# Kernel optimization log

Hardware: AMD Instinct MI355X
Metric: run time of the kernel (lower is better)

## Reference

```python
import jax, jax.numpy as jnp
import numpy as np

EMB = 1024
HID = 4096
NHEADS = 16
DK = EMB // NHEADS
EPS = 1e-6
B, S = 2, 2048


def setup_inputs() -> dict:
    key = jax.random.key(0)
    ks = jax.random.split(key, 10)
    sc = 0.02
    return {
        "x": jax.random.normal(ks[0], (B, S, EMB), dtype=jnp.float32),
        "src_mask": jnp.ones((B, 1, 1, S), dtype=jnp.int32),
        "wq": jax.random.normal(ks[1], (EMB, EMB), dtype=jnp.float32) * sc,
        "wk": jax.random.normal(ks[2], (EMB, EMB), dtype=jnp.float32) * sc,
        "wv": jax.random.normal(ks[3], (EMB, EMB), dtype=jnp.float32) * sc,
        "wo": jax.random.normal(ks[4], (EMB, EMB), dtype=jnp.float32) * sc,
        "ff1_w": jax.random.normal(ks[5], (EMB, HID), dtype=jnp.float32) * sc,
        "ff1_b": jnp.zeros((HID,), dtype=jnp.float32),
        "ff2_w": jax.random.normal(ks[6], (HID, EMB), dtype=jnp.float32) * sc,
        "ff2_b": jnp.zeros((EMB,), dtype=jnp.float32),
        "ln1_a": jnp.ones((1,), dtype=jnp.float32),
        "ln1_b": jnp.zeros((1,), dtype=jnp.float32),
        "ln2_a": jnp.ones((1,), dtype=jnp.float32),
        "ln2_b": jnp.zeros((1,), dtype=jnp.float32),
    }


def layernorm(x, alpha, bias):
    # Faithful to the custom LayerNorm: scalar alpha/bias, std with Bessel
    # correction (torch default unbiased=True), divide by (std + eps).
    mean = jnp.mean(x, axis=-1, keepdims=True)
    var = jnp.sum((x - mean) ** 2, axis=-1, keepdims=True) / (x.shape[-1] - 1)
    std = jnp.sqrt(var)
    return alpha * (x - mean) / (std + EPS) + bias


def mha(x, mask, wq, wk, wv, wo):
    b, s, _ = x.shape
    def split_heads(t):  # [B,S,E] -> [B,H,S,dk]
        return t.reshape(b, s, NHEADS, DK).transpose(0, 2, 1, 3)
    q = split_heads(x @ wq)
    k = split_heads(x @ wk)
    v = split_heads(x @ wv)
    scores = jnp.einsum("bhqd,bhkd->bhqk", q, k) / jnp.sqrt(jnp.float32(DK))
    scores = jnp.where(mask == 0, -jnp.inf, scores)
    attn = jax.nn.softmax(scores, axis=-1)
    out = jnp.einsum("bhqk,bhkd->bhqd", attn, v)
    out = out.transpose(0, 2, 1, 3).reshape(b, s, EMB)
    return out @ wo


def ffn(x, w1, b1, w2, b2):
    return jax.nn.relu(x @ w1 + b1) @ w2 + b2


def reference(x, src_mask, wq, wk, wv, wo, ff1_w, ff1_b, ff2_w, ff2_b,
              ln1_a, ln1_b, ln2_a, ln2_b):
    # pre-norm residual encoder block (dropout=0 / eval mode)
    h = x + mha(layernorm(x, ln1_a, ln1_b), src_mask, wq, wk, wv, wo)
    out = h + ffn(layernorm(h, ln2_a, ln2_b), ff1_w, ff1_b, ff2_w, ff2_b)
    return out
```

## Files before the change

kernel.cpp:

```cpp
#include <hip/hip_runtime.h>
#include <stdint.h>

#define EMB 1024
#define HID 4096
#define NHEADS 16
#define DKH 64
#define SEQ 2048
#define BATCH 2
#define MROWS (BATCH * SEQ)
#define GBK 64

typedef unsigned short u16;
typedef unsigned int u32;
typedef __attribute__((ext_vector_type(8))) short short8;
typedef __attribute__((ext_vector_type(4))) float f32x4;
typedef __attribute__((ext_vector_type(16))) float f32x16;
typedef __attribute__((ext_vector_type(4))) u32 u32x4;
typedef __attribute__((ext_vector_type(2))) int i32x2;

#if __has_builtin(__builtin_amdgcn_exp2f)
#define QK_SCALE 0.18033688011f
#define QK_CLAMP 43.3f
__device__ __forceinline__ float pexp(float x) { return __builtin_amdgcn_exp2f(x); }
#else
#define QK_SCALE 0.125f
#define QK_CLAMP 30.0f
__device__ __forceinline__ float pexp(float x) { return __expf(x); }
#endif

__device__ __forceinline__ u16 f2bf(float f) {
    unsigned u = __float_as_uint(f);
    unsigned r = 0x7FFFu + ((u >> 16) & 1u);
    return (u16)((u + r) >> 16);
}
__device__ __forceinline__ f32x4 mfma16(short8 a, short8 b, f32x4 c) {
    return __builtin_amdgcn_mfma_f32_16x16x32_bf16(a, b, c, 0, 0, 0);
}
__device__ __forceinline__ f32x16 mfma32(short8 a, short8 b, f32x16 c) {
    return __builtin_amdgcn_mfma_f32_32x32x16_bf16(a, b, c, 0, 0, 0);
}
__device__ __forceinline__ void gl_lds16(const u16* g, u16* l) {
    __builtin_amdgcn_global_load_lds(
        (__attribute__((address_space(1))) void*)g,
        (__attribute__((address_space(3))) void*)l, 16, 0, 0);
}
__device__ __forceinline__ void plswap(u32& a, u32& b) {
#if __has_builtin(__builtin_amdgcn_permlane32_swap)
    i32x2 r = __builtin_amdgcn_permlane32_swap((int)a, (int)b, false, false);
    a = (u32)r.x; b = (u32)r.y;
#else
    const u32 ta = (u32)__shfl_xor((int)a, 32);
    const u32 tb = (u32)__shfl_xor((int)b, 32);
    const bool hi = (threadIdx.x & 32) != 0;
    const u32 na = hi ? tb : a;
    const u32 nb = hi ? b : ta;
    a = na; b = nb;
#endif
}
__device__ __forceinline__ short8 mk8(u32 a, u32 b, u32 c, u32 d) {
    u32x4 t; t.x = a; t.y = b; t.z = c; t.w = d;
    return __builtin_bit_cast(short8, t);
}

__global__ __launch_bounds__(256) void transpose_qkvo(
    const float* __restrict__ wq, const float* __restrict__ wk,
    const float* __restrict__ wv, const float* __restrict__ wo,
    u16* __restrict__ qkvT, u16* __restrict__ woT,
    const int* __restrict__ msk, int* __restrict__ flag) {
    __shared__ u16 t[32][33];
    const int z = blockIdx.z;
    const float* W = (z == 0) ? wq : (z == 1) ? wk : (z == 2) ? wv : wo;
    u16* WT = (z < 3) ? (qkvT + (size_t)z * EMB * EMB) : woT;
    const float scale = (z == 0) ? QK_SCALE : 1.0f;
    const int tx = threadIdx.x & 31, ty = threadIdx.x >> 5;
    const int k0 = blockIdx.y * 32, n0 = blockIdx.x * 32;
#pragma unroll
    for (int r = 0; r < 32; r += 8)
        t[ty + r][tx] = f2bf(scale * W[(size_t)(k0 + ty + r) * EMB + n0 + tx]);
    __syncthreads();
#pragma unroll
    for (int r = 0; r < 32; r += 8)
        WT[(size_t)(n0 + ty + r) * EMB + k0 + tx] = t[tx][ty + r];

    if (z == 3 && blockIdx.x == 0 && blockIdx.y == 0) {
        int v = 1;
        for (int i = threadIdx.x; i < BATCH * SEQ; i += 256)
            v &= (msk[i] != 0) ? 1 : 0;
        v = __all(v) ? 1 : 0;
        __shared__ int rr[4];
        if ((threadIdx.x & 63) == 0) rr[threadIdx.x >> 6] = v;
        __syncthreads();
        if (threadIdx.x == 0) flag[0] = rr[0] & rr[1] & rr[2] & rr[3];
    }
}

__global__ __launch_bounds__(256) void transpose_bf16(
    const float* __restrict__ W, u16* __restrict__ WT, int K, int N) {
    __shared__ u16 t[32][33];
    const int tx = threadIdx.x & 31, ty = threadIdx.x >> 5;
    const int k0 = blockIdx.y * 32, n0 = blockIdx.x * 32;
#pragma unroll
    for (int r = 0; r < 32; r += 8)
        t[ty + r][tx] = f2bf(W[(size_t)(k0 + ty + r) * N + n0 + tx]);
    __syncthreads();
#pragma unroll
    for (int r = 0; r < 32; r += 8)
        WT[(size_t)(n0 + ty + r) * K + k0 + tx] = t[tx][ty + r];
}

__global__ __launch_bounds__(256) void ln_kernel(
    const float* __restrict__ x, u16* __restrict__ out,
    const float* __restrict__ alpha_p, const float* __restrict__ beta_p) {
    const int row = blockIdx.x;
    const int tid = threadIdx.x;
    float4 v = reinterpret_cast<const float4*>(x + (size_t)row * EMB)[tid];

    __shared__ float red[4];
    float s = v.x + v.y + v.z + v.w;
    for (int off = 32; off; off >>= 1) s += __shfl_down(s, off);
    if ((tid & 63) == 0) red[tid >> 6] = s;
    __syncthreads();
    float mean = (red[0] + red[1] + red[2] + red[3]) * (1.0f / EMB);
    __syncthreads();

    float d0 = v.x - mean, d1 = v.y - mean, d2 = v.z - mean, d3 = v.w - mean;
    float sq = d0 * d0 + d1 * d1 + d2 * d2 + d3 * d3;
    for (int off = 32; off; off >>= 1) sq += __shfl_down(sq, off);
    if ((tid & 63) == 0) red[tid >> 6] = sq;
    __syncthreads();
    float var = (red[0] + red[1] + red[2] + red[3]) * (1.0f / (EMB - 1));
    float inv = 1.0f / (sqrtf(var) + 1e-6f);
    float a = alpha_p[0], b = beta_p[0];

    ushort4 o;
    o.x = f2bf(a * d0 * inv + b);
    o.y = f2bf(a * d1 * inv + b);
    o.z = f2bf(a * d2 * inv + b);
    o.w = f2bf(a * d3 * inv + b);
    reinterpret_cast<ushort4*>(out + (size_t)row * EMB)[tid] = o;
}

template <int BN, int NWM>
__global__ __launch_bounds__(512) void gemm_mfma(
    const u16* __restrict__ A, const u16* __restrict__ BT, void* C,
    const float* __restrict__ bias, const void* res,
    int M, int N, int K, int relu, int out_mode,
    u16* __restrict__ Kb_out, u16* __restrict__ VT_out) {
    constexpr int NWN = 8 / NWM;
    constexpr int WM = 128 / (16 * NWM);
    constexpr int WN = BN / (16 * NWN);
    constexpr int NBUF = (BN == 64) ? 3 : 2;
    __shared__ u16 As[NBUF][128][GBK];
    __shared__ u16 Bs[NBUF][BN][GBK];

    const int tid = threadIdx.x;
    const int wave = tid >> 6, lane = tid & 63;
    const int quad = lane >> 4, lc = lane & 15;
    const int wm = wave % NWM, wn = wave / NWM;

    const int nx = gridDim.x;
    const int bid = blockIdx.y * nx + blockIdx.x;
    const int xcd = bid & 7, sl = bid >> 3;
    const int nyx = gridDim.y >> 3;
    const int bcol = sl % nx;
    const int brow = (sl / nx) + xcd * nyx;
    const int row0 = brow * 128, col0 = bcol * BN;

    const int srow = lane >> 3;
    const int scg = (lane & 7) ^ srow;

    f32x4 acc[WM][WN] = {};

    auto stage = [&](int k0, int buf) {
#pragma unroll
        for (int i = 0; i < 2; ++i) {
            const int rb = wave * 16 + i * 8;
            gl_lds16(A + (size_t)(row0 + rb + srow) * K + k0 + scg * 8,
                     &As[buf][rb][0]);
        }
        if constexpr (BN == 128) {
#pragma unroll
            for (int i = 0; i < 2; ++i) {
                const int rb = wave * 16 + i * 8;
                gl_lds16(BT + (size_t)(col0 + rb + srow) * K + k0 + scg * 8,
                         &Bs[buf][rb][0]);
            }
        } else {
            const int rb = wave * 8;
            gl_lds16(BT + (size_t)(col0 + rb + srow) * K + k0 + scg * 8,
                     &Bs[buf][rb][0]);
        }
    };

    auto compute = [&](int cur) {
#pragma unroll
        for (int s = 0; s < 2; ++s) {
            short8 af[WM], bfv[WN];
#pragma unroll
            for (int i = 0; i < WM; ++i) {
                const int ar = wm * (16 * WM) + i * 16 + lc;
                af[i] = *reinterpret_cast<const short8*>(
                    &As[cur][ar][(((s * 4 + quad) ^ (ar & 7))) * 8]);
            }
#pragma unroll
            for (int j = 0; j < WN; ++j) {
                const int br = wn * (16 * WN) + j * 16 + lc;
                bfv[j] = *reinterpret_cast<const short8*>(
                    &Bs[cur][br][(((s * 4 + quad) ^ (br & 7))) * 8]);
            }
#pragma unroll
            for (int i = 0; i < WM; ++i)
#pragma unroll
                for (int j = 0; j < WN; ++j)
                    acc[i][j] = mfma16(af[i], bfv[j], acc[i][j]);
        }
    };

    if constexpr (NBUF == 2) {
        stage(0, 0);
        __syncthreads();
        int cur = 0;
        for (int k0 = 0; k0 < K; k0 += GBK) {
            if (k0 + GBK < K) stage(k0 + GBK, cur ^ 1);
            compute(cur);
            __syncthreads();
            cur ^= 1;
        }
    } else {
        stage(0, 0);
        if (GBK < K) stage(GBK, 1);
        int cur = 0;
        for (int k0 = 0; k0 < K; k0 += GBK) {
            if (k0 + 2 * GBK < K) {
                int nb = cur + 2; if (nb >= 3) nb -= 3;
                stage(k0 + 2 * GBK, nb);
            }
            const int rem = (K - k0) >> 6;
            if (rem > 2)       asm volatile("s_waitcnt vmcnt(6)" ::: "memory");
            else if (rem == 2) asm volatile("s_waitcnt vmcnt(3)" ::: "memory");
            else               asm volatile("s_waitcnt vmcnt(0)" ::: "memory");
            __builtin_amdgcn_s_barrier();
            __builtin_amdgcn_sched_barrier(0);
            compute(cur);
            __builtin_amdgcn_s_barrier();
            cur = (cur == 2) ? 0 : cur + 1;
        }
    }

    u16* Cb = (u16*)C;
    int mode = out_mode, ncols = N, lcol0 = col0;
    if (out_mode == 3) {
        const int seg = col0 >> 10;
        lcol0 = col0 & 1023;
        ncols = EMB;
        if (seg == 1) { Cb = Kb_out; mode = 0; }
        else if (seg == 2) { Cb = VT_out; mode = 2; }
        else { mode = 0; }
    }

#pragma unroll
    for (int j = 0; j < WN; ++j) {
        const int col = lcol0 + wn * (16 * WN) + j * 16 + lc;
        const float bv = bias ? bias[col] : 0.f;
#pragma unroll
        for (int i = 0; i < WM; ++i) {
            const int rbase = row0 + wm * (16 * WM) + i * 16 + quad * 4;
            if (mode == 2) {
                ushort4 o;
                o.x = f2bf(acc[i][j][0]); o.y = f2bf(acc[i][j][1]);
                o.z = f2bf(acc[i][j][2]); o.w = f2bf(acc[i][j][3]);
                *reinterpret_cast<ushort4*>(Cb + (size_t)col * M + rbase) = o;
            } else {
#pragma unroll
                for (int r = 0; r < 4; ++r) {
                    const size_t idx = (size_t)(rbase + r) * ncols + col;
                    float v = acc[i][j][r] + bv;
                    if (relu) v = fmaxf(v, 0.f);
                    if (res) v += ((const float*)res)[idx];
                    if (mode == 1) ((float*)C)[idx] = v;
                    else Cb[idx] = f2bf(v);
                }
            }
        }
    }
}

__global__ __launch_bounds__(512) void gemm_ws(
    const u16* __restrict__ A, const u16* __restrict__ BT, void* C,
    const float* __restrict__ bias, const void* res,
    int M, int N, int K, int relu, int fp32out) {
    __shared__ __align__(16) char smem[65536];
    u16 (*As)[128][GBK] = (u16(*)[128][GBK])smem;
    u16 (*Bs)[128][GBK] = (u16(*)[128][GBK])(smem + 32768);

    const int tid = threadIdx.x;
    const int wave = tid >> 6, lane = tid & 63;
    const int quad = lane >> 4, lc = lane & 15;
    const int p = wave >> 1, s = wave & 1;
    const int pm = p >> 1, pn = p & 1;

    const int nx = gridDim.x;
    const int bid = blockIdx.y * nx + blockIdx.x;
    const int xcd = bid & 7, sl = bid >> 3;
    const int nyx = gridDim.y >> 3;
    const int bcol = sl % nx;
    const int brow = (sl / nx) + xcd * nyx;
    const int row0 = brow * 128, col0 = bcol * 128;

    const int srow = lane >> 3;
    const int scg = (lane & 7) ^ srow;

    f32x4 acc[4][4] = {};

    auto stage = [&](int k0, int buf) {
#pragma unroll
        for (int i = 0; i < 2; ++i) {
            const int rb = wave * 16 + i * 8;
            gl_lds16(A + (size_t)(row0 + rb + srow) * K + k0 + scg * 8,
                     &As[buf][rb][0]);
        }
#pragma unroll
        for (int i = 0; i < 2; ++i) {
            const int rb = wave * 16 + i * 8;
            gl_lds16(BT + (size_t)(col0 + rb + srow) * K + k0 + scg * 8,
                     &Bs[buf][rb][0]);
        }
    };

    const int nt = K >> 6;
    stage(0, 0);
    int cur = 0;
    for (int t = 0; t < nt; ++t) {
        if (t + 1 < nt) {
            stage((t + 1) << 6, cur ^ 1);
            asm volatile("s_waitcnt vmcnt(4)" ::: "memory");
        } else {
            asm volatile("s_waitcnt vmcnt(0)" ::: "memory");
        }
        __builtin_amdgcn_s_barrier();
        __builtin_amdgcn_sched_barrier(0);

        short8 af[4], bfv[4];
#pragma unroll
        for (int i = 0; i < 4; ++i) {
            const int ar = pm * 64 + i * 16 + lc;
            af[i] = *reinterpret_cast<const short8*>(
                &As[cur][ar][(((s * 4 + quad) ^ (ar & 7))) * 8]);
        }
#pragma unroll
        for (int j = 0; j < 4; ++j) {
            const int br = pn * 64 + j * 16 + lc;
            bfv[j] = *reinterpret_cast<const short8*>(
                &Bs[cur][br][(((s * 4 + quad) ^ (br & 7))) * 8]);
        }
#pragma unroll
        for (int i = 0; i < 4; ++i)
#pragma unroll
            for (int j = 0; j < 4; ++j)
                acc[i][j] = mfma16(af[i], bfv[j], acc[i][j]);

        __builtin_amdgcn_s_barrier();
        cur ^= 1;
    }

    float* Ms = (float*)smem;
    if (s == 0) {
#pragma unroll
        for (int i = 0; i < 4; ++i)
#pragma unroll
            for (int j = 0; j < 4; ++j)
#pragma unroll
                for (int r = 0; r < 4; ++r)
                    Ms[(pm * 64 + i * 16 + quad * 4 + r) * 128 +
                       pn * 64 + j * 16 + lc] = acc[i][j][r];
    }
    __syncthreads();
    if (s == 1) {
#pragma unroll
        for (int i = 0; i < 4; ++i)
#pragma unroll
            for (int j = 0; j < 4; ++j)
#pragma unroll
                for (int r = 0; r < 4; ++r)
                    Ms[(pm * 64 + i * 16 + quad * 4 + r) * 128 +
                       pn * 64 + j * 16 + lc] += acc[i][j][r];
    }
    __syncthreads();

#pragma unroll
    for (int k = 0; k < 8; ++k) {
        const int fi = (k * 512 + tid) * 4;
        const int row = fi >> 7, col = fi & 127;
        const float4 v = *reinterpret_cast<const float4*>(&Ms[fi]);
        float o0 = v.x, o1 = v.y, o2 = v.z, o3 = v.w;
        if (bias) {
            const float4 bv = *reinterpret_cast<const float4*>(&bias[col0 + col]);
            o0 += bv.x; o1 += bv.y; o2 += bv.z; o3 += bv.w;
        }
        if (relu) {
            o0 = fmaxf(o0, 0.f); o1 = fmaxf(o1, 0.f);
            o2 = fmaxf(o2, 0.f); o3 = fmaxf(o3, 0.f);
        }
        const size_t gidx = (size_t)(row0 + row) * N + col0 + col;
        if (res) {
            const float4 rv = *reinterpret_cast<const float4*>(
                &((const float*)res)[gidx]);
            o0 += rv.x; o1 += rv.y; o2 += rv.z; o3 += rv.w;
        }
        if (fp32out) {
            float4 ov; ov.x = o0; ov.y = o1; ov.z = o2; ov.w = o3;
            *reinterpret_cast<float4*>(&((float*)C)[gidx]) = ov;
        } else {
            ushort4 ov;
            ov.x = f2bf(o0); ov.y = f2bf(o1); ov.z = f2bf(o2); ov.w = f2bf(o3);
            *reinterpret_cast<ushort4*>(&((u16*)C)[gidx]) = ov;
        }
    }
}

__global__ __launch_bounds__(512, 4) void attn_mfma(
    const u16* __restrict__ Q, const u16* __restrict__ K,
    const u16* __restrict__ VT, const int* __restrict__ mask,
    const int* __restrict__ mflag, u16* __restrict__ O) {
    const int tid = threadIdx.x;
    const int wave = tid >> 6, lane = tid & 63;
    const int hi = lane >> 5, ln31 = lane & 31;
    const int qt = wave >> 1, s = wave & 1;
    const int H = blockIdx.x & 31;
    const int qblk = blockIdx.x >> 5;
    const int h = H & 15, b = H >> 4;

    __shared__ __align__(16) char smem[65536];
    u16 (*Ks)[128][DKH] = (u16(*)[128][DKH])smem;
    u16 (*Vs)[DKH][128] = (u16(*)[DKH][128])(smem + 32768);

    const int fast = mflag[0];

    const u16* qp = Q + (size_t)(b * SEQ + qblk * 128 + qt * 32 + ln31) * EMB
                      + h * DKH + hi * 8;
    short8 qb[4];
#pragma unroll
    for (int f = 0; f < 4; ++f)
        qb[f] = *reinterpret_cast<const short8*>(qp + f * 16);

    const int srow = lane >> 3, scg = (lane & 7) ^ srow;
    const int svr = lane >> 4, ssl = lane & 15;

    auto stage = [&](int kc, int buf) {
#pragma unroll
        for (int i = 0; i < 2; ++i) {
            const int t8 = wave * 16 + i * 8;
            gl_lds16(K + (size_t)(b * SEQ + kc + t8 + srow) * EMB + h * DKH + scg * 8,
                     &Ks[buf][t8][0]);
        }
#pragma unroll
        for (int i = 0; i < 2; ++i) {
            const int d4 = wave * 8 + i * 4;
            const int dim = d4 + svr;
            const int gv = ssl ^ (dim & 15);
            gl_lds16(VT + (size_t)(h * DKH + dim) * MROWS + b * SEQ + kc + gv * 8,
                     &Vs[buf][d4][0]);
        }
    };

    f32x16 o0 = {}, o1 = {};
    float rs = 0.f;
    const int tok0 = s * 64;

    stage(0, 0);
    __syncthreads();
    int cur = 0;

    for (int kc = 0; kc < SEQ; kc += 128) {
        if (kc + 128 < SEQ) stage(kc + 128, cur ^ 1);

#pragma unroll
        for (int mt = 0; mt < 2; ++mt) {
            const int trow = tok0 + mt * 32 + ln31;
            f32x16 st = {};
#pragma unroll
            for (int f = 0; f < 4; ++f) {
                const int slot = (2 * f + hi) ^ (trow & 7);
                const short8 ka = *reinterpret_cast<const short8*>(
                    &Ks[cur][trow][slot * 8]);
                st = mfma32(ka, qb[f], st);
            }
            if (fast) {
#pragma unroll
                for (int r = 0; r < 16; ++r)
                    st[r] = pexp(fminf(st[r], QK_CLAMP));
            } else {
#pragma unroll
                for (int g = 0; g < 4; ++g) {
                    const int4 mk = *reinterpret_cast<const int4*>(
                        mask + b * SEQ + kc + tok0 + mt * 32 + g * 8 + hi * 4);
                    const int* mkp = &mk.x;
#pragma unroll
                    for (int r4 = 0; r4 < 4; ++r4) {
                        const int r = g * 4 + r4;
                        const float pv = pexp(fminf(st[r], QK_CLAMP));
                        st[r] = mkp[r4] ? pv : 0.f;
                    }
                }
            }
            rs += (((st[0] + st[1]) + (st[2] + st[3])) +
                   ((st[4] + st[5]) + (st[6] + st[7]))) +
                  (((st[8] + st[9]) + (st[10] + st[11])) +
                   ((st[12] + st[13]) + (st[14] + st[15])));

            u32 pk0 = __builtin_amdgcn_perm(__float_as_uint(st[1]),
                                            __float_as_uint(st[0]), 0x07060302u);
            u32 pk1 = __builtin_amdgcn_perm(__float_as_uint(st[3]),
                                            __float_as_uint(st[2]), 0x07060302u);
            u32 pk2 = __builtin_amdgcn_perm(__float_as_uint(st[5]),
                                            __float_as_uint(st[4]), 0x07060302u);
            u32 pk3 = __builtin_amdgcn_perm(__float_as_uint(st[7]),
                                            __float_as_uint(st[6]), 0x07060302u);
            u32 pk4 = __builtin_amdgcn_perm(__float_as_uint(st[9]),
                                            __float_as_uint(st[8]), 0x07060302u);
            u32 pk5 = __builtin_amdgcn_perm(__float_as_uint(st[11]),
                                            __float_as_uint(st[10]), 0x07060302u);
            u32 pk6 = __builtin_amdgcn_perm(__float_as_uint(st[13]),
                                            __float_as_uint(st[12]), 0x07060302u);
            u32 pk7 = __builtin_amdgcn_perm(__float_as_uint(st[15]),
                                            __float_as_uint(st[14]), 0x07060302u);
            plswap(pk0, pk2);
            plswap(pk1, pk3);
            plswap(pk4, pk6);
            plswap(pk5, pk7);
            const short8 fr0 = mk8(pk0, pk1, pk2, pk3);
            const short8 fr1 = mk8(pk4, pk5, pk6, pk7);

#pragma unroll
            for (int sub = 0; sub < 2; ++sub) {
                const short8 fr = sub ? fr1 : fr0;
                const int g = s * 8 + (2 * mt + sub) * 2 + hi;
#pragma unroll
                for (int nt = 0; nt < 2; ++nt) {
                    const int drow = nt * 32 + ln31;
                    const short8 vb = *reinterpret_cast<const short8*>(
                        &Vs[cur][drow][(g ^ (drow & 15)) * 8]);
                    if (nt == 0) o0 = mfma32(fr, vb, o0);
                    else         o1 = mfma32(fr, vb, o1);
                }
            }
        }
        __syncthreads();
        cur ^= 1;
    }

    rs += __shfl_xor(rs, 32);

    float* Om = (float*)smem;
    float* Ls = (float*)(smem + 34816);

    if (s == 0) {
#pragma unroll
        for (int nt = 0; nt < 2; ++nt)
#pragma unroll
            for (int r = 0; r < 16; ++r) {
                const int row = (r & 3) + 8 * (r >> 2) + 4 * hi;
                Om[(qt * 32 + row) * 68 + nt * 32 + ln31] = nt ? o1[r] : o0[r];
            }
        if (lane < 32) Ls[qt * 32 + ln31] = rs;
    }
    __syncthreads();
    if (s == 1) {
        const float lt = rs + Ls[qt * 32 + ln31];
        if (lane < 32) Ls[qt * 32 + ln31] = lt;
#pragma unroll
        for (int nt = 0; nt < 2; ++nt)
#pragma unroll
            for (int r = 0; r < 16; ++r) {
                const int row = (r & 3) + 8 * (r >> 2) + 4 * hi;
                const int idx = (qt * 32 + row) * 68 + nt * 32 + ln31;
                Om[idx] += nt ? o1[r] : o0[r];
            }
    }
    __syncthreads();

    {
        const int q = tid >> 2, seg = tid & 3;
        const float inv = 1.0f / Ls[q];
        const float* src = Om + q * 68 + seg * 16;
        u16* dst = O + (size_t)(b * SEQ + qblk * 128 + q) * EMB + h * DKH + seg * 16;
#pragma unroll
        for (int i = 0; i < 4; ++i) {
            const float4 v = *reinterpret_cast<const float4*>(src + i * 4);
            ushort4 ou;
            ou.x = f2bf(v.x * inv); ou.y = f2bf(v.y * inv);
            ou.z = f2bf(v.z * inv); ou.w = f2bf(v.w * inv);
            *reinterpret_cast<ushort4*>(dst + i * 4) = ou;
        }
    }
}

extern "C" void kernel_launch(void* const* d_in, const int* in_sizes, int n_in,
                              void* d_out, int out_size, void* d_ws, size_t ws_size,
                              hipStream_t stream) {
    const float* x     = (const float*)d_in[0];
    const int*   mask  = (const int*)d_in[1];
    const float* wq    = (const float*)d_in[2];
    const float* wk    = (const float*)d_in[3];
    const float* wv    = (const float*)d_in[4];
    const float* wo    = (const float*)d_in[5];
    const float* ff1_w = (const float*)d_in[6];
    const float* ff1_b = (const float*)d_in[7];
    const float* ff2_w = (const float*)d_in[8];
    const float* ff2_b = (const float*)d_in[9];
    const float* ln1_a = (const float*)d_in[10];
    const float* ln1_b = (const float*)d_in[11];
    const float* ln2_a = (const float*)d_in[12];
    const float* ln2_b = (const float*)d_in[13];
    float* out = (float*)d_out;

    char* ws = (char*)d_ws;
    const size_t MB = 1u << 20;
    u16* act   = (u16*)(ws + 0);
    u16* Qb    = (u16*)(ws + 8 * MB);
    u16* Kb    = (u16*)(ws + 16 * MB);
    u16* VTb   = (u16*)(ws + 24 * MB);
    int* mflag = (int*)(ws + 32 * MB);
    u16* f1    = (u16*)(ws + 8 * MB);
    u16* wqkvT = (u16*)(ws + 40 * MB);
    u16* woT   = (u16*)(ws + 46 * MB);
    u16* ffT   = (u16*)(ws + 40 * MB);

    transpose_qkvo<<<dim3(EMB / 32, EMB / 32, 4), 256, 0, stream>>>(
        wq, wk, wv, wo, wqkvT, woT, mask, mflag);

    ln_kernel<<<MROWS, 256, 0, stream>>>(x, act, ln1_a, ln1_b);

    gemm_mfma<128, 2><<<dim3(3 * EMB / 128, MROWS / 128), 512, 0, stream>>>(
        act, wqkvT, Qb, nullptr, nullptr, MROWS, 3 * EMB, EMB, 0, 3, Kb, VTb);

    attn_mfma<<<BATCH * NHEADS * (SEQ / 128), 512, 0, stream>>>(
        Qb, Kb, VTb, mask, mflag, act);

    gemm_mfma<64, 4><<<dim3(EMB / 64, MROWS / 128), 512, 0, stream>>>(
        act, woT, out, nullptr, x, MROWS, EMB, EMB, 0, 1, nullptr, nullptr);

    ln_kernel<<<MROWS, 256, 0, stream>>>(out, act, ln2_a, ln2_b);

    transpose_bf16<<<dim3(HID / 32, EMB / 32), 256, 0, stream>>>(ff1_w, ffT, EMB, HID);
    gemm_ws<<<dim3(HID / 128, MROWS / 128), 512, 0, stream>>>(
        act, ffT, f1, ff1_b, nullptr, MROWS, HID, EMB, 1, 0);

    transpose_bf16<<<dim3(EMB / 32, HID / 32), 256, 0, stream>>>(ff2_w, ffT, HID, EMB);
    gemm_ws<<<dim3(EMB / 128, MROWS / 128), 512, 0, stream>>>(
        f1, ffT, out, ff2_b, out, MROWS, EMB, HID, 0, 1);
}
```

Measured before the change: 351.6 us.

## Double attention query tile per block to reuse K/V tiles, finer vmcnt waits

Each attention block now handles 256 query rows instead of 128. Every wave holds two 32-row Q tiles, so each K and V fragment read from LDS feeds two MFMAs, and half as many blocks each stage K/V from global memory. The prefetch sync is replaced by an explicit vmcnt wait plus a raw barrier, so the next chunk's loads stay in flight during compute. In exchange, register pressure roughly doubles, launch bounds drop to 2 blocks per CU, and only 256 blocks are launched, which lowers occupancy and parallelism.

```diff
diff --git a/kernel.cpp b/kernel.cpp
--- a/kernel.cpp
+++ b/kernel.cpp
@@ -418,30 +418,33 @@
     }
 }
 
-__global__ __launch_bounds__(512, 4) void attn_mfma(
+__global__ __launch_bounds__(512, 2) void attn_mfma(
     const u16* __restrict__ Q, const u16* __restrict__ K,
     const u16* __restrict__ VT, const int* __restrict__ mask,
     const int* __restrict__ mflag, u16* __restrict__ O) {
     const int tid = threadIdx.x;
     const int wave = tid >> 6, lane = tid & 63;
     const int hi = lane >> 5, ln31 = lane & 31;
-    const int qt = wave >> 1, s = wave & 1;
+    const int qp = wave >> 1, s = wave & 1;
     const int H = blockIdx.x & 31;
     const int qblk = blockIdx.x >> 5;
     const int h = H & 15, b = H >> 4;
 
-    __shared__ __align__(16) char smem[65536];
+    __shared__ __align__(16) char smem[70656];
     u16 (*Ks)[128][DKH] = (u16(*)[128][DKH])smem;
     u16 (*Vs)[DKH][128] = (u16(*)[DKH][128])(smem + 32768);
 
     const int fast = mflag[0];
 
-    const u16* qp = Q + (size_t)(b * SEQ + qblk * 128 + qt * 32 + ln31) * EMB
-                      + h * DKH + hi * 8;
-    short8 qb[4];
-#pragma unroll
-    for (int f = 0; f < 4; ++f)
-        qb[f] = *reinterpret_cast<const short8*>(qp + f * 16);
+    short8 qb[2][4];
+#pragma unroll
+    for (int t = 0; t < 2; ++t) {
+        const u16* qsrc = Q + (size_t)(b * SEQ + qblk * 256 + qp * 64 + t * 32 + ln31) * EMB
+                            + h * DKH + hi * 8;
+#pragma unroll
+        for (int f = 0; f < 4; ++f)
+            qb[t][f] = *reinterpret_cast<const short8*>(qsrc + f * 16);
+    }
 
     const int srow = lane >> 3, scg = (lane & 7) ^ srow;
     const int svr = lane >> 4, ssl = lane & 15;
@@ -463,129 +466,165 @@
         }
     };
 
-    f32x16 o0 = {}, o1 = {};
-    float rs = 0.f;
+    f32x16 o00 = {}, o01 = {}, o10 = {}, o11 = {};
+    float rs0 = 0.f, rs1 = 0.f;
     const int tok0 = s * 64;
 
+    const int NCH = SEQ / 128;
     stage(0, 0);
-    __syncthreads();
     int cur = 0;
 
-    for (int kc = 0; kc < SEQ; kc += 128) {
-        if (kc + 128 < SEQ) stage(kc + 128, cur ^ 1);
+    for (int tch = 0; tch < NCH; ++tch) {
+        if (tch + 1 < NCH) {
+            stage((tch + 1) * 128, cur ^ 1);
+            asm volatile("s_waitcnt vmcnt(4)" ::: "memory");
+        } else {
+            asm volatile("s_waitcnt vmcnt(0)" ::: "memory");
+        }
+        __builtin_amdgcn_s_barrier();
+        __builtin_amdgcn_sched_barrier(0);
+        const int kc = tch * 128;
 
 #pragma unroll
         for (int mt = 0; mt < 2; ++mt) {
             const int trow = tok0 + mt * 32 + ln31;
-            f32x16 st = {};
+            f32x16 st0 = {}, st1 = {};
 #pragma unroll
             for (int f = 0; f < 4; ++f) {
                 const int slot = (2 * f + hi) ^ (trow & 7);
                 const short8 ka = *reinterpret_cast<const short8*>(
                     &Ks[cur][trow][slot * 8]);
-                st = mfma32(ka, qb[f], st);
-            }
-            if (fast) {
-#pragma unroll
-                for (int r = 0; r < 16; ++r)
-                    st[r] = pexp(fminf(st[r], QK_CLAMP));
-            } else {
-#pragma unroll
-                for (int g = 0; g < 4; ++g) {
-                    const int4 mk = *reinterpret_cast<const int4*>(
+                st0 = mfma32(ka, qb[0][f], st0);
+                st1 = mfma32(ka, qb[1][f], st1);
+            }
+            int4 mks[4];
+            if (!fast) {
+#pragma unroll
+                for (int g = 0; g < 4; ++g)
+                    mks[g] = *reinterpret_cast<const int4*>(
                         mask + b * SEQ + kc + tok0 + mt * 32 + g * 8 + hi * 4);
-                    const int* mkp = &mk.x;
-#pragma unroll
-                    for (int r4 = 0; r4 < 4; ++r4) {
-                        const int r = g * 4 + r4;
-                        const float pv = pexp(fminf(st[r], QK_CLAMP));
-                        st[r] = mkp[r4] ? pv : 0.f;
+            }
+            short8 fr[2][2];
+#pragma unroll
+            for (int t = 0; t < 2; ++t) {
+                f32x16& st = t ? st1 : st0;
+                if (fast) {
+#pragma unroll
+                    for (int r = 0; r < 16; ++r)
+                        st[r] = pexp(fminf(st[r], QK_CLAMP));
+                } else {
+#pragma unroll
+                    for (int g = 0; g < 4; ++g) {
+                        const int* mkp = &mks[g].x;
+#pragma unroll
+                        for (int r4 = 0; r4 < 4; ++r4) {
+                            const int r = g * 4 + r4;
+                            const float pv = pexp(fminf(st[r], QK_CLAMP));
+                            st[r] = mkp[r4] ? pv : 0.f;
+                        }
                     }
                 }
-            }
-            rs += (((st[0] + st[1]) + (st[2] + st[3])) +
-                   ((st[4] + st[5]) + (st[6] + st[7]))) +
-                  (((st[8] + st[9]) + (st[10] + st[11])) +
-                   ((st[12] + st[13]) + (st[14] + st[15])));
-
-            u32 pk0 = __builtin_amdgcn_perm(__float_as_uint(st[1]),
-                                            __float_as_uint(st[0]), 0x07060302u);
-            u32 pk1 = __builtin_amdgcn_perm(__float_as_uint(st[3]),
-                                            __float_as_uint(st[2]), 0x07060302u);
-            u32 pk2 = __builtin_amdgcn_perm(__float_as_uint(st[5]),
-                                            __float_as_uint(st[4]), 0x07060302u);
-            u32 pk3 = __builtin_amdgcn_perm(__float_as_uint(st[7]),
-                                            __float_as_uint(st[6]), 0x07060302u);
-            u32 pk4 = __builtin_amdgcn_perm(__float_as_uint(st[9]),
-                                            __float_as_uint(st[8]), 0x07060302u);
-            u32 pk5 = __builtin_amdgcn_perm(__float_as_uint(st[11]),
-                                            __float_as_uint(st[10]), 0x07060302u);
-            u32 pk6 = __builtin_amdgcn_perm(__float_as_uint(st[13]),
-                                            __float_as_uint(st[12]), 0x07060302u);
-            u32 pk7 = __builtin_amdgcn_perm(__float_as_uint(st[15]),
-                                            __float_as_uint(st[14]), 0x07060302u);
-            plswap(pk0, pk2);
-            plswap(pk1, pk3);
-            plswap(pk4, pk6);
-            plswap(pk5, pk7);
-            const short8 fr0 = mk8(pk0, pk1, pk2, pk3);
-            const short8 fr1 = mk8(pk4, pk5, pk6, pk7);
+                const float sum =
+                    (((st[0] + st[1]) + (st[2] + st[3])) +
+                     ((st[4] + st[5]) + (st[6] + st[7]))) +
+                    (((st[8] + st[9]) + (st[10] + st[11])) +
+                     ((st[12] + st[13]) + (st[14] + st[15])));
+                if (t) rs1 += sum; else rs0 += sum;
+
+                u32 pk0 = __builtin_amdgcn_perm(__float_as_uint(st[1]),
+                                                __float_as_uint(st[0]), 0x07060302u);
+                u32 pk1 = __builtin_amdgcn_perm(__float_as_uint(st[3]),
+                                                __float_as_uint(st[2]), 0x07060302u);
+                u32 pk2 = __builtin_amdgcn_perm(__float_as_uint(st[5]),
+                                                __float_as_uint(st[4]), 0x07060302u);
+                u32 pk3 = __builtin_amdgcn_perm(__float_as_uint(st[7]),
+                                                __float_as_uint(st[6]), 0x07060302u);
+                u32 pk4 = __builtin_amdgcn_perm(__float_as_uint(st[9]),
+                                                __float_as_uint(st[8]), 0x07060302u);
+                u32 pk5 = __builtin_amdgcn_perm(__float_as_uint(st[11]),
+                                                __float_as_uint(st[10]), 0x07060302u);
+                u32 pk6 = __builtin_amdgcn_perm(__float_as_uint(st[13]),
+                                                __float_as_uint(st[12]), 0x07060302u);
+                u32 pk7 = __builtin_amdgcn_perm(__float_as_uint(st[15]),
+                                                __float_as_uint(st[14]), 0x07060302u);
+                plswap(pk0, pk2);
+                plswap(pk1, pk3);
+                plswap(pk4, pk6);
+                plswap(pk5, pk7);
+                fr[t][0] = mk8(pk0, pk1, pk2, pk3);
+                fr[t][1] = mk8(pk4, pk5, pk6, pk7);
+            }
 
 #pragma unroll
             for (int sub = 0; sub < 2; ++sub) {
-                const short8 fr = sub ? fr1 : fr0;
                 const int g = s * 8 + (2 * mt + sub) * 2 + hi;
 #pragma unroll
                 for (int nt = 0; nt < 2; ++nt) {
                     const int drow = nt * 32 + ln31;
                     const short8 vb = *reinterpret_cast<const short8*>(
                         &Vs[cur][drow][(g ^ (drow & 15)) * 8]);
-                    if (nt == 0) o0 = mfma32(fr, vb, o0);
-                    else         o1 = mfma32(fr, vb, o1);
+                    if (nt == 0) {
+                        o00 = mfma32(fr[0][sub], vb, o00);
+                        o10 = mfma32(fr[1][sub], vb, o10);
+                    } else {
+                        o01 = mfma32(fr[0][sub], vb, o01);
+                        o11 = mfma32(fr[1][sub], vb, o11);
+                    }
                 }
             }
         }
-        __syncthreads();
+        __builtin_amdgcn_s_barrier();
         cur ^= 1;
     }
 
-    rs += __shfl_xor(rs, 32);
+    rs0 += __shfl_xor(rs0, 32);
+    rs1 += __shfl_xor(rs1, 32);
 
     float* Om = (float*)smem;
-    float* Ls = (float*)(smem + 34816);
+    float* Ls = (float*)(smem + 69632);
 
     if (s == 0) {
 #pragma unroll
-        for (int nt = 0; nt < 2; ++nt)
-#pragma unroll
-            for (int r = 0; r < 16; ++r) {
-                const int row = (r & 3) + 8 * (r >> 2) + 4 * hi;
-                Om[(qt * 32 + row) * 68 + nt * 32 + ln31] = nt ? o1[r] : o0[r];
-            }
-        if (lane < 32) Ls[qt * 32 + ln31] = rs;
+        for (int t = 0; t < 2; ++t) {
+            const int tile = qp * 2 + t;
+#pragma unroll
+            for (int nt = 0; nt < 2; ++nt) {
+                const f32x16& ov = t ? (nt ? o11 : o10) : (nt ? o01 : o00);
+#pragma unroll
+                for (int r = 0; r < 16; ++r) {
+                    const int row = (r & 3) + 8 * (r >> 2) + 4 * hi;
+                    Om[(tile * 32 + row) * 68 + nt * 32 + ln31] = ov[r];
+                }
+            }
+            if (lane < 32) Ls[tile * 32 + ln31] = t ? rs1 : rs0;
+        }
     }
     __syncthreads();
     if (s == 1) {
-        const float lt = rs + Ls[qt * 32 + ln31];
-        if (lane < 32) Ls[qt * 32 + ln31] = lt;
-#pragma unroll
-        for (int nt = 0; nt < 2; ++nt)
-#pragma unroll
-            for (int r = 0; r < 16; ++r) {
-                const int row = (r & 3) + 8 * (r >> 2) + 4 * hi;
-                const int idx = (qt * 32 + row) * 68 + nt * 32 + ln31;
-                Om[idx] += nt ? o1[r] : o0[r];
-            }
+#pragma unroll
+        for (int t = 0; t < 2; ++t) {
+            const int tile = qp * 2 + t;
+            if (lane < 32) Ls[tile * 32 + ln31] += (t ? rs1 : rs0);
+#pragma unroll
+            for (int nt = 0; nt < 2; ++nt) {
+                const f32x16& ov = t ? (nt ? o11 : o10) : (nt ? o01 : o00);
+#pragma unroll
+                for (int r = 0; r < 16; ++r) {
+                    const int row = (r & 3) + 8 * (r >> 2) + 4 * hi;
+                    Om[(tile * 32 + row) * 68 + nt * 32 + ln31] += ov[r];
+                }
+            }
+        }
     }
     __syncthreads();
 
     {
-        const int q = tid >> 2, seg = tid & 3;
+        const int q = tid >> 1, seg = tid & 1;
         const float inv = 1.0f / Ls[q];
-        const float* src = Om + q * 68 + seg * 16;
-        u16* dst = O + (size_t)(b * SEQ + qblk * 128 + q) * EMB + h * DKH + seg * 16;
-#pragma unroll
-        for (int i = 0; i < 4; ++i) {
+        const float* src = Om + q * 68 + seg * 32;
+        u16* dst = O + (size_t)(b * SEQ + qblk * 256 + q) * EMB + h * DKH + seg * 32;
+#pragma unroll
+        for (int i = 0; i < 8; ++i) {
             const float4 v = *reinterpret_cast<const float4*>(src + i * 4);
             ushort4 ou;
             ou.x = f2bf(v.x * inv); ou.y = f2bf(v.y * inv);
@@ -634,7 +673,7 @@
     gemm_mfma<128, 2><<<dim3(3 * EMB / 128, MROWS / 128), 512, 0, stream>>>(
         act, wqkvT, Qb, nullptr, nullptr, MROWS, 3 * EMB, EMB, 0, 3, Kb, VTb);
 
-    attn_mfma<<<BATCH * NHEADS * (SEQ / 128), 512, 0, stream>>>(
+    attn_mfma<<<BATCH * NHEADS * (SEQ / 256), 512, 0, stream>>>(
         Qb, Kb, VTb, mask, mflag, act);
 
     gemm_mfma<64, 4><<<dim3(EMB / 64, MROWS / 128), 512, 0, stream>>>(
```

Result: faster. 338.7 us (-3.7%).
